# Kernel optimization log

Measured on AMD Instinct MI355X. Metric: run time of the kernel, lower is better.

## Reference

```python
import jax, jax.numpy as jnp
import numpy as np

D = 768
ED = 192  # d // 4
E = 8     # n_experts
K = 2     # top_k
B, H, W = 32, 32, 32
LN_EPS = 1e-5


def setup_inputs() -> dict:
    key = jax.random.key(0)
    ks = jax.random.split(key, 5)
    s = 0.02
    x = jax.random.normal(ks[0], (B, D, H, W), dtype=jnp.float32)
    Wr = jax.random.normal(ks[1], (E, D), dtype=jnp.float32) * s   # router: logits = tokens @ Wr.T
    W1 = jax.random.normal(ks[2], (E, D, ED), dtype=jnp.float32) * s  # gate proj (silu branch)
    W3 = jax.random.normal(ks[3], (E, D, ED), dtype=jnp.float32) * s  # linear branch
    W2 = jax.random.normal(ks[4], (E, ED, D), dtype=jnp.float32) * s  # down proj
    gamma = jnp.ones((D,), dtype=jnp.float32)
    beta = jnp.zeros((D,), dtype=jnp.float32)
    return {"x": x, "Wr": Wr, "W1": W1, "W3": W3, "W2": W2, "gamma": gamma, "beta": beta}


def _layernorm(y, gamma, beta):
    mu = jnp.mean(y, axis=-1, keepdims=True)
    var = jnp.mean(jnp.square(y - mu), axis=-1, keepdims=True)
    return (y - mu) * jax.lax.rsqrt(var + LN_EPS) * gamma + beta


def _moe_forward(x, Wr, W1, W3, W2, gamma, beta):
    b, c, h, w = x.shape
    tokens = x.transpose(0, 2, 3, 1).reshape(-1, c)        # [T, d]
    logits = tokens @ Wr.T                                  # [T, E]
    topk_v, topk_i = jax.lax.top_k(logits, K)               # [T, K]
    topk_w = jax.nn.softmax(topk_v, axis=-1)                # [T, K]
    # dense combine weights: zero for non-selected experts (same math as masked scatter)
    gates = jnp.sum(jax.nn.one_hot(topk_i, E, dtype=tokens.dtype) * topk_w[..., None], axis=1)  # [T, E]
    # SwiGLU per expert (forward uses silu(e[0](t)) * e[2](t), then e[3])
    hdn = jax.nn.silu(jnp.einsum('td,edh->teh', tokens, W1)) * jnp.einsum('td,edh->teh', tokens, W3)  # [T,E,ed]
    y = jnp.einsum('te,teh,ehd->td', gates, hdn, W2)        # combine: [T, d]
    out = _layernorm(y, gamma, beta) + tokens
    return out.reshape(b, h, w, c).transpose(0, 3, 1, 2)


def reference(x, Wr, W1, W3, W2, gamma, beta):
    return _moe_forward(x, Wr, W1, W3, W2, gamma, beta)
```

## Files before the change

kernel.cpp:

```cpp
#include <hip/hip_runtime.h>
#include <cstdint>
#include <cstddef>

#define T_TOK 32768
#define DM 768
#define EDIM 192
#define NEXP 8

typedef unsigned short u16;
typedef short bf16x8 __attribute__((ext_vector_type(8)));
typedef float f32x4 __attribute__((ext_vector_type(4)));
typedef u16 u16x8 __attribute__((ext_vector_type(8)));

__device__ __forceinline__ u16 f2bf(float f) {
  unsigned u = __float_as_uint(f);
  return (u16)((u + 0x7FFFu + ((u >> 16) & 1u)) >> 16);
}
__device__ __forceinline__ float bf2f(u16 u) {
  return __uint_as_float(((unsigned)u) << 16);
}

__device__ __forceinline__ bf16x8 frag_ld(const u16* lds, int row, int kb) {
  int ph = row * 128 + (kb ^ ((row & 7) << 4));
  return *(const bf16x8*)((const char*)lds + ph);
}

__global__ __launch_bounds__(256) void k_prep(
    const float* __restrict__ W1, const float* __restrict__ W3,
    const float* __restrict__ W2, u16* __restrict__ W1T,
    u16* __restrict__ W3T, u16* __restrict__ W2T)
{
  __shared__ __align__(16) float td[64][68];
  const int z = blockIdx.z;
  const int mat = z >> 3, e = z & 7;
  const int R = (mat == 2) ? EDIM : DM;
  const int C = (mat == 2) ? DM : EDIM;
  const int r0 = blockIdx.x * 64, c0 = blockIdx.y * 64;
  if (r0 >= R || c0 >= C) return;
  const float* in = (mat == 0 ? W1 : mat == 1 ? W3 : W2) + (size_t)e * R * C;
  u16* out = (mat == 0 ? W1T : mat == 1 ? W3T : W2T) + (size_t)e * R * C;
  const int tid = threadIdx.x;
  {
    int rl = tid >> 2, cs = (tid & 3) * 16;
    const float* s = in + (size_t)(r0 + rl) * C + c0 + cs;
    #pragma unroll
    for (int i = 0; i < 16; i += 4) *(float4*)&td[rl][cs + i] = *(const float4*)(s + i);
  }
  __syncthreads();
  {
    int cl = tid >> 2, rs = (tid & 3) * 16;
    u16* d = out + (size_t)(c0 + cl) * R + r0 + rs;
    u16x8 o0, o1;
    #pragma unroll
    for (int i = 0; i < 8; ++i) {
      o0[i] = f2bf(td[rs + i][cl]);
      o1[i] = f2bf(td[rs + 8 + i][cl]);
    }
    *(u16x8*)d = o0;
    *(u16x8*)(d + 8) = o1;
  }
}

__global__ __launch_bounds__(256) void k_tokrouter(
    const float* __restrict__ x, const float* __restrict__ Wr,
    u16* __restrict__ tokbf, int* __restrict__ cnt,
    int* __restrict__ toklist, float* __restrict__ gatelist)
{
  __shared__ __align__(16) float tokL[64][64];
  __shared__ float WrL[8][64];
  __shared__ float logitsL[64][8];
  __shared__ int cnt8[8];
  __shared__ int baseL[8];
  const int tid = threadIdx.x;
  const int t0 = blockIdx.x * 64;
  const int b = t0 >> 10;
  const int h0 = (t0 >> 5) & 31;
  const float* xb = x + (size_t)b * (DM * 1024);

  const int tr = tid & 63;
  const int ep = tid >> 6;
  float l0 = 0.f, l1 = 0.f;

  for (int cb = 0; cb < 12; ++cb) {
    const int c0 = cb * 64;
    __syncthreads();
    {
      int f = tid;
      #pragma unroll
      for (int it = 0; it < 2; ++it, f += 256)
        WrL[f >> 6][f & 63] = Wr[(f >> 6) * DM + c0 + (f & 63)];
    }
    {
      int cl = tid >> 2;
      int ts = (tid & 3) * 16;
      int hh = h0 + (ts >> 5), ww = ts & 31;
      const float* src = xb + ((size_t)(c0 + cl) * 32 + hh) * 32 + ww;
      float* d = &tokL[cl][ts];
      #pragma unroll
      for (int i = 0; i < 16; i += 4) *(float4*)(d + i) = *(const float4*)(src + i);
    }
    __syncthreads();
    for (int c = 0; c < 64; ++c) {
      float tv = tokL[c][tr];
      l0 = fmaf(tv, WrL[ep][c], l0);
      l1 = fmaf(tv, WrL[ep + 4][c], l1);
    }
    {
      int tl = tid >> 2;
      int cs = (tid & 3) * 16;
      u16x8 o0, o1;
      #pragma unroll
      for (int i = 0; i < 8; ++i) {
        o0[i] = f2bf(tokL[cs + i][tl]);
        o1[i] = f2bf(tokL[cs + 8 + i][tl]);
      }
      u16* d = tokbf + (size_t)(t0 + tl) * DM + c0 + cs;
      *(u16x8*)d = o0;
      *(u16x8*)(d + 8) = o1;
    }
  }

  logitsL[tr][ep] = l0;
  logitsL[tr][ep + 4] = l1;
  if (tid < 8) cnt8[tid] = 0;
  __syncthreads();

  int e0 = -1, e1 = -1, lp0 = 0, lp1 = 0;
  float g0 = 0.f, g1 = 0.f;
  if (tid < 64) {
    float v0 = -1e30f, v1 = -1e30f;
    #pragma unroll
    for (int e = 0; e < 8; ++e) { float v = logitsL[tid][e]; if (v > v0) { v0 = v; e0 = e; } }
    #pragma unroll
    for (int e = 0; e < 8; ++e) {
      if (e == e0) continue;
      float v = logitsL[tid][e]; if (v > v1) { v1 = v; e1 = e; }
    }
    float w = expf(v1 - v0);
    g0 = 1.f / (1.f + w);
    g1 = w / (1.f + w);
    lp0 = atomicAdd(&cnt8[e0], 1);
    lp1 = atomicAdd(&cnt8[e1], 1);
  }
  __syncthreads();
  if (tid < 8) baseL[tid] = atomicAdd(&cnt[tid], cnt8[tid]);
  __syncthreads();
  if (tid < 64) {
    int tg = t0 + tid;
    int p0 = baseL[e0] + lp0;
    int p1 = baseL[e1] + lp1;
    toklist[e0 * T_TOK + p0] = tg;
    gatelist[e0 * T_TOK + p0] = g0;
    toklist[e1 * T_TOK + p1] = tg | (1 << 16);
    gatelist[e1 * T_TOK + p1] = g1;
  }
}

__global__ void k_prefix(const int* __restrict__ cnt, int* __restrict__ offs) {
  if (threadIdx.x == 0) {
    int s = 0;
    for (int e = 0; e < NEXP; ++e) { offs[e] = s; s += cnt[e]; }
    offs[NEXP] = s;
  }
}

__global__ __launch_bounds__(256) void k_ffn1(
    const u16* __restrict__ tokbf, const u16* __restrict__ W1T,
    const u16* __restrict__ W3T, const int* __restrict__ cnt,
    const int* __restrict__ offs, const int* __restrict__ toklist,
    u16* __restrict__ hbuf)
{
  __shared__ __align__(16) u16 As[128 * 64];
  __shared__ __align__(16) u16 B1s[64 * 64];
  __shared__ __align__(16) u16 B3s[64 * 64];
  __shared__ int rowbaseL[128];
  const int e = blockIdx.z;
  const int count = cnt[e];
  const int start = blockIdx.x * 128;
  if (start >= count) return;
  const int n0 = blockIdx.y * 64;
  const int rows = min(128, count - start);
  const int tid = threadIdx.x;

  if (tid < 128) {
    int r = (tid < rows) ? tid : 0;
    rowbaseL[tid] = (toklist[e * T_TOK + start + r] & 0xFFFF) * DM;
  }
  __syncthreads();

  const int w = tid >> 6, l = tid & 63;
  const int wm = (w >> 1) * 64, wn = (w & 1) * 32;
  const int lr = l & 15;
  const int lk = (l >> 4) * 16;

  f32x4 acc1[4][2], acc3[4][2];
  #pragma unroll
  for (int i = 0; i < 4; ++i)
    #pragma unroll
    for (int j = 0; j < 2; ++j) {
      acc1[i][j] = (f32x4){0.f, 0.f, 0.f, 0.f};
      acc3[i][j] = (f32x4){0.f, 0.f, 0.f, 0.f};
    }

  for (int kc = 0; kc < 12; ++kc) {
    #pragma unroll
    for (int it = 0; it < 4; ++it) {
      int idx = it * 256 + tid;
      int r = idx >> 3, s = idx & 7;
      int sw = (s * 16) ^ ((r & 7) << 4);
      const u16* src = tokbf + rowbaseL[r] + kc * 64 + (sw >> 1);
      *(u16x8*)((char*)As + idx * 16) = *(const u16x8*)src;
    }
    #pragma unroll
    for (int it = 0; it < 2; ++it) {
      int idx = it * 256 + tid;
      int r = idx >> 3, s = idx & 7;
      int sw = (s * 16) ^ ((r & 7) << 4);
      size_t wb = (size_t)(e * EDIM + n0 + r) * DM + kc * 64 + (sw >> 1);
      *(u16x8*)((char*)B1s + idx * 16) = *(const u16x8*)(W1T + wb);
      *(u16x8*)((char*)B3s + idx * 16) = *(const u16x8*)(W3T + wb);
    }
    __syncthreads();
    #pragma unroll
    for (int kk = 0; kk < 2; ++kk) {
      const int kb = kk * 64 + lk;
      bf16x8 af[4], b1[2], b3[2];
      #pragma unroll
      for (int mf = 0; mf < 4; ++mf) af[mf] = frag_ld(As, wm + mf * 16 + lr, kb);
      #pragma unroll
      for (int nf = 0; nf < 2; ++nf) {
        b1[nf] = frag_ld(B1s, wn + nf * 16 + lr, kb);
        b3[nf] = frag_ld(B3s, wn + nf * 16 + lr, kb);
      }
      #pragma unroll
      for (int mf = 0; mf < 4; ++mf)
        #pragma unroll
        for (int nf = 0; nf < 2; ++nf) {
          acc1[mf][nf] = __builtin_amdgcn_mfma_f32_16x16x32_bf16(af[mf], b1[nf], acc1[mf][nf], 0, 0, 0);
          acc3[mf][nf] = __builtin_amdgcn_mfma_f32_16x16x32_bf16(af[mf], b3[nf], acc3[mf][nf], 0, 0, 0);
        }
    }
    __syncthreads();
  }

  const int rq = (l >> 4) * 4;
  const int abase = offs[e] + start;
  #pragma unroll
  for (int mf = 0; mf < 4; ++mf)
    #pragma unroll
    for (int nf = 0; nf < 2; ++nf)
      #pragma unroll
      for (int r = 0; r < 4; ++r) {
        int m = wm + mf * 16 + rq + r;
        if (m < rows) {
          float a = acc1[mf][nf][r];
          float hv = (a / (1.f + expf(-a))) * acc3[mf][nf][r];
          hbuf[(size_t)(abase + m) * EDIM + (n0 + wn + nf * 16 + lr)] = f2bf(hv);
        }
      }
}

__global__ __launch_bounds__(256) void k_ffn2(
    const u16* __restrict__ hbuf, const u16* __restrict__ W2T,
    const int* __restrict__ cnt, const int* __restrict__ offs,
    const int* __restrict__ toklist, const float* __restrict__ gatelist,
    u16* __restrict__ ypart)
{
  __shared__ __align__(16) u16 As[128 * 64];
  __shared__ __align__(16) u16 Bs[128 * 64];
  __shared__ int dstL[128];
  __shared__ float gL[128];
  const int e = blockIdx.z;
  const int count = cnt[e];
  const int start = blockIdx.x * 128;
  if (start >= count) return;
  const int n0 = blockIdx.y * 128;
  const int rows = min(128, count - start);
  const int tid = threadIdx.x;
  const int abase = offs[e] + start;

  if (tid < 128) {
    int r = (tid < rows) ? tid : 0;
    int entry = toklist[e * T_TOK + start + r];
    int t = entry & 0xFFFF, k = entry >> 16;
    dstL[tid] = (k * T_TOK + t) * DM;
    gL[tid] = gatelist[e * T_TOK + start + r];
  }
  __syncthreads();

  const int w = tid >> 6, l = tid & 63;
  const int wm = (w >> 1) * 64, wn = (w & 1) * 64;
  const int lr = l & 15;
  const int lk = (l >> 4) * 16;

  f32x4 acc[4][4];
  #pragma unroll
  for (int i = 0; i < 4; ++i)
    #pragma unroll
    for (int j = 0; j < 4; ++j) acc[i][j] = (f32x4){0.f, 0.f, 0.f, 0.f};

  for (int kc = 0; kc < 3; ++kc) {
    #pragma unroll
    for (int it = 0; it < 4; ++it) {
      int idx = it * 256 + tid;
      int r = idx >> 3, s = idx & 7;
      int sw = (s * 16) ^ ((r & 7) << 4);
      int rr = (r < rows) ? r : 0;
      const u16* sa = hbuf + (size_t)(abase + rr) * EDIM + kc * 64 + (sw >> 1);
      *(u16x8*)((char*)As + idx * 16) = *(const u16x8*)sa;
      const u16* sb = W2T + (size_t)(e * DM + n0 + r) * EDIM + kc * 64 + (sw >> 1);
      *(u16x8*)((char*)Bs + idx * 16) = *(const u16x8*)sb;
    }
    __syncthreads();
    #pragma unroll
    for (int kk = 0; kk < 2; ++kk) {
      const int kb = kk * 64 + lk;
      bf16x8 af[4], bf_[4];
      #pragma unroll
      for (int mf = 0; mf < 4; ++mf) af[mf] = frag_ld(As, wm + mf * 16 + lr, kb);
      #pragma unroll
      for (int nf = 0; nf < 4; ++nf) bf_[nf] = frag_ld(Bs, wn + nf * 16 + lr, kb);
      #pragma unroll
      for (int mf = 0; mf < 4; ++mf)
        #pragma unroll
        for (int nf = 0; nf < 4; ++nf)
          acc[mf][nf] = __builtin_amdgcn_mfma_f32_16x16x32_bf16(af[mf], bf_[nf], acc[mf][nf], 0, 0, 0);
    }
    __syncthreads();
  }

  const int rq = (l >> 4) * 4;
  #pragma unroll
  for (int mf = 0; mf < 4; ++mf)
    #pragma unroll
    for (int nf = 0; nf < 4; ++nf)
      #pragma unroll
      for (int r = 0; r < 4; ++r) {
        int m = wm + mf * 16 + rq + r;
        if (m < rows) {
          float v = acc[mf][nf][r] * gL[m];
          ypart[(size_t)dstL[m] + (n0 + wn + nf * 16 + lr)] = f2bf(v);
        }
      }
}

__global__ __launch_bounds__(256) void k_ln(
    const u16* __restrict__ ypart, const float* __restrict__ x,
    const float* __restrict__ gamma, const float* __restrict__ beta,
    float* __restrict__ out)
{
  __shared__ float lnT[64][65];
  __shared__ float muL[64], rsL[64];
  const int tid = threadIdx.x;
  const int t0 = blockIdx.x * 64;
  const int b = t0 >> 10;
  const int h0 = (t0 >> 5) & 31;
  const u16* y0 = ypart;
  const u16* y1 = ypart + (size_t)T_TOK * DM;
  const int tl = tid >> 2, q = tid & 3;
  const size_t tbase = (size_t)(t0 + tl) * DM;

  float sum = 0.f, sq = 0.f;
  for (int jj = 0; jj < 12; ++jj) {
    int c = jj * 64 + q * 16;
    u16x8 a0 = *(const u16x8*)(y0 + tbase + c);
    u16x8 a1 = *(const u16x8*)(y0 + tbase + c + 8);
    u16x8 b0 = *(const u16x8*)(y1 + tbase + c);
    u16x8 b1 = *(const u16x8*)(y1 + tbase + c + 8);
    #pragma unroll
    for (int i = 0; i < 8; ++i) {
      float v = bf2f(a0[i]) + bf2f(b0[i]); sum += v; sq += v * v;
      float u = bf2f(a1[i]) + bf2f(b1[i]); sum += u; sq += u * u;
    }
  }
  sum += __shfl_xor(sum, 1); sq += __shfl_xor(sq, 1);
  sum += __shfl_xor(sum, 2); sq += __shfl_xor(sq, 2);
  float mu = sum * (1.f / 768.f);
  float var = sq * (1.f / 768.f) - mu * mu;
  float rs = 1.0f / sqrtf(var + 1e-5f);
  if (q == 0) { muL[tl] = mu; rsL[tl] = rs; }
  __syncthreads();

  for (int cb = 0; cb < 12; ++cb) {
    const int c0 = cb * 64;
    if (cb) __syncthreads();
    {
      float mu_ = muL[tl], rs_ = rsL[tl];
      int c = c0 + q * 16;
      u16x8 a0 = *(const u16x8*)(y0 + tbase + c);
      u16x8 a1 = *(const u16x8*)(y0 + tbase + c + 8);
      u16x8 b0 = *(const u16x8*)(y1 + tbase + c);
      u16x8 b1 = *(const u16x8*)(y1 + tbase + c + 8);
      #pragma unroll
      for (int i = 0; i < 8; ++i) {
        float v = bf2f(a0[i]) + bf2f(b0[i]);
        lnT[q * 16 + i][tl] = (v - mu_) * rs_ * gamma[c + i] + beta[c + i];
        float u = bf2f(a1[i]) + bf2f(b1[i]);
        lnT[q * 16 + 8 + i][tl] = (u - mu_) * rs_ * gamma[c + 8 + i] + beta[c + 8 + i];
      }
    }
    __syncthreads();
    {
      int cl = tid >> 2, ts = (tid & 3) * 16;
      int c = c0 + cl;
      int hh = h0 + (ts >> 5), ww = ts & 31;
      size_t oidx = (((size_t)b * DM + c) * 32 + hh) * 32 + ww;
      #pragma unroll
      for (int i = 0; i < 16; i += 4) {
        float4 xv = *(const float4*)(x + oidx + i);
        float4 ov;
        ov.x = lnT[cl][ts + i + 0] + xv.x;
        ov.y = lnT[cl][ts + i + 1] + xv.y;
        ov.z = lnT[cl][ts + i + 2] + xv.z;
        ov.w = lnT[cl][ts + i + 3] + xv.w;
        *(float4*)(out + oidx + i) = ov;
      }
    }
  }
}

constexpr size_t OFF_TOK  = 0;
constexpr size_t OFF_W1T  = OFF_TOK + (size_t)T_TOK * DM * 2;
constexpr size_t OFF_W3T  = OFF_W1T + (size_t)NEXP * EDIM * DM * 2;
constexpr size_t OFF_W2T  = OFF_W3T + (size_t)NEXP * EDIM * DM * 2;
constexpr size_t OFF_H    = OFF_W2T + (size_t)NEXP * EDIM * DM * 2;
constexpr size_t OFF_YP   = OFF_H + (size_t)T_TOK * 2 * EDIM * 2;
constexpr size_t OFF_CNT  = OFF_YP + (size_t)2 * T_TOK * DM * 2;
constexpr size_t OFF_OFFS = OFF_CNT + 256;
constexpr size_t OFF_LIST = OFF_OFFS + 256;
constexpr size_t OFF_GATE = OFF_LIST + (size_t)NEXP * T_TOK * 4;

extern "C" void kernel_launch(void* const* d_in, const int* in_sizes, int n_in,
                              void* d_out, int out_size, void* d_ws, size_t ws_size,
                              hipStream_t stream) {
  const float* x     = (const float*)d_in[0];
  const float* Wr    = (const float*)d_in[1];
  const float* W1    = (const float*)d_in[2];
  const float* W3    = (const float*)d_in[3];
  const float* W2    = (const float*)d_in[4];
  const float* gamma = (const float*)d_in[5];
  const float* beta  = (const float*)d_in[6];
  float* out = (float*)d_out;
  char* ws = (char*)d_ws;

  u16* tokbf = (u16*)(ws + OFF_TOK);
  u16* W1T   = (u16*)(ws + OFF_W1T);
  u16* W3T   = (u16*)(ws + OFF_W3T);
  u16* W2T   = (u16*)(ws + OFF_W2T);
  u16* hbuf  = (u16*)(ws + OFF_H);
  u16* ypart = (u16*)(ws + OFF_YP);
  int* cnt   = (int*)(ws + OFF_CNT);
  int* offs  = (int*)(ws + OFF_OFFS);
  int* toklist = (int*)(ws + OFF_LIST);
  float* gatelist = (float*)(ws + OFF_GATE);

  hipMemsetAsync(cnt, 0, 64, stream);
  hipLaunchKernelGGL(k_prep, dim3(12, 12, 24), dim3(256), 0, stream,
                     W1, W3, W2, W1T, W3T, W2T);
  hipLaunchKernelGGL(k_tokrouter, dim3(512), dim3(256), 0, stream,
                     x, Wr, tokbf, cnt, toklist, gatelist);
  hipLaunchKernelGGL(k_prefix, dim3(1), dim3(64), 0, stream, cnt, offs);
  hipLaunchKernelGGL(k_ffn1, dim3(256, 3, 8), dim3(256), 0, stream,
                     tokbf, W1T, W3T, cnt, offs, toklist, hbuf);
  hipLaunchKernelGGL(k_ffn2, dim3(256, 6, 8), dim3(256), 0, stream,
                     hbuf, W2T, cnt, offs, toklist, gatelist, ypart);
  hipLaunchKernelGGL(k_ln, dim3(512), dim3(256), 0, stream,
                     ypart, x, gamma, beta, out);
}
```

Baseline: 246.6 us.

## Use direct global-to-LDS loads in FFN GEMMs and split router and layernorm for parallelism

The FFN1 and FFN2 GEMM tile loads now use global_load_lds, which writes global memory straight into LDS without passing through registers, and source pointers are computed once outside the k-loop. The router kernel now handles 32 tokens per block (twice as many blocks), keeps all of Wr in LDS, and gives each thread one (token, expert) logit. The layernorm is split into a per-token stats kernel and a 2D-grid apply kernel so more blocks run in parallel. The cost is an extra launch and an extra read of ypart, and the direct LDS loads depend on the swizzled layout matching the lane-ordered writes.

```diff
diff --git a/kernel.cpp b/kernel.cpp
--- a/kernel.cpp
+++ b/kernel.cpp
@@ -18,6 +18,13 @@
 }
 __device__ __forceinline__ float bf2f(u16 u) {
   return __uint_as_float(((unsigned)u) << 16);
+}
+
+__device__ __forceinline__ void gld16(const void* g, void* l) {
+  __builtin_amdgcn_global_load_lds(
+      (const __attribute__((address_space(1))) unsigned int*)g,
+      (__attribute__((address_space(3))) unsigned int*)l,
+      16, 0, 0);
 }
 
 __device__ __forceinline__ bf16x8 frag_ld(const u16* lds, int row, int kb) {
@@ -66,68 +73,58 @@
     u16* __restrict__ tokbf, int* __restrict__ cnt,
     int* __restrict__ toklist, float* __restrict__ gatelist)
 {
-  __shared__ __align__(16) float tokL[64][64];
-  __shared__ float WrL[8][64];
-  __shared__ float logitsL[64][8];
+  __shared__ float WrL[8][772];
+  __shared__ float xL[64][33];
+  __shared__ float logitsL[32][8];
   __shared__ int cnt8[8];
   __shared__ int baseL[8];
   const int tid = threadIdx.x;
-  const int t0 = blockIdx.x * 64;
+  const int t0 = blockIdx.x * 32;
   const int b = t0 >> 10;
-  const int h0 = (t0 >> 5) & 31;
-  const float* xb = x + (size_t)b * (DM * 1024);
-
-  const int tr = tid & 63;
-  const int ep = tid >> 6;
-  float l0 = 0.f, l1 = 0.f;
+  const int h = (t0 >> 5) & 31;
+  const float* xb = x + (size_t)b * (DM * 1024) + h * 32;
+
+  for (int i = tid; i < 1536; i += 256) {
+    int r = i / 192;
+    int c = (i - r * 192) * 4;
+    *(float4*)&WrL[r][c] = ((const float4*)Wr)[i];
+  }
+
+  const int rt = tid >> 3;
+  const int re = tid & 7;
+  float lacc = 0.f;
 
   for (int cb = 0; cb < 12; ++cb) {
     const int c0 = cb * 64;
     __syncthreads();
+    #pragma unroll
+    for (int it = 0; it < 2; ++it) {
+      int idx = it * 256 + tid;
+      int r = idx >> 3, cc = (idx & 7) * 4;
+      float4 v = *(const float4*)(xb + (size_t)(c0 + r) * 1024 + cc);
+      xL[r][cc] = v.x; xL[r][cc + 1] = v.y; xL[r][cc + 2] = v.z; xL[r][cc + 3] = v.w;
+    }
+    __syncthreads();
     {
-      int f = tid;
-      #pragma unroll
-      for (int it = 0; it < 2; ++it, f += 256)
-        WrL[f >> 6][f & 63] = Wr[(f >> 6) * DM + c0 + (f & 63)];
+      const float* wr = &WrL[re][c0];
+      #pragma unroll
+      for (int c = 0; c < 64; ++c) lacc = fmaf(xL[c][rt], wr[c], lacc);
     }
     {
-      int cl = tid >> 2;
-      int ts = (tid & 3) * 16;
-      int hh = h0 + (ts >> 5), ww = ts & 31;
-      const float* src = xb + ((size_t)(c0 + cl) * 32 + hh) * 32 + ww;
-      float* d = &tokL[cl][ts];
-      #pragma unroll
-      for (int i = 0; i < 16; i += 4) *(float4*)(d + i) = *(const float4*)(src + i);
-    }
-    __syncthreads();
-    for (int c = 0; c < 64; ++c) {
-      float tv = tokL[c][tr];
-      l0 = fmaf(tv, WrL[ep][c], l0);
-      l1 = fmaf(tv, WrL[ep + 4][c], l1);
-    }
-    {
-      int tl = tid >> 2;
-      int cs = (tid & 3) * 16;
-      u16x8 o0, o1;
-      #pragma unroll
-      for (int i = 0; i < 8; ++i) {
-        o0[i] = f2bf(tokL[cs + i][tl]);
-        o1[i] = f2bf(tokL[cs + 8 + i][tl]);
-      }
-      u16* d = tokbf + (size_t)(t0 + tl) * DM + c0 + cs;
-      *(u16x8*)d = o0;
-      *(u16x8*)(d + 8) = o1;
-    }
-  }
-
-  logitsL[tr][ep] = l0;
-  logitsL[tr][ep + 4] = l1;
+      u16x8 o;
+      #pragma unroll
+      for (int i = 0; i < 8; ++i) o[i] = f2bf(xL[re * 8 + i][rt]);
+      *(u16x8*)(tokbf + (size_t)(t0 + rt) * DM + c0 + re * 8) = o;
+    }
+  }
+
+  logitsL[rt][re] = lacc;
   if (tid < 8) cnt8[tid] = 0;
   __syncthreads();
 
   int e0 = -1, e1 = -1, lp0 = 0, lp1 = 0;
   float g0 = 0.f, g1 = 0.f;
-  if (tid < 64) {
+  if (tid < 32) {
     float v0 = -1e30f, v1 = -1e30f;
     #pragma unroll
     for (int e = 0; e < 8; ++e) { float v = logitsL[tid][e]; if (v > v0) { v0 = v; e0 = e; } }
@@ -145,7 +142,7 @@
   __syncthreads();
   if (tid < 8) baseL[tid] = atomicAdd(&cnt[tid], cnt8[tid]);
   __syncthreads();
-  if (tid < 64) {
+  if (tid < 32) {
     int tg = t0 + tid;
     int p0 = baseL[e0] + lp0;
     int p1 = baseL[e1] + lp1;
@@ -188,6 +185,19 @@
   }
   __syncthreads();
 
+  const int lrow = tid >> 3;
+  const int swq = (((tid & 7) * 16) ^ ((lrow & 7) << 4)) >> 1;
+  const u16 *srcA[4], *srcB1[2], *srcB3[2];
+  #pragma unroll
+  for (int it = 0; it < 4; ++it)
+    srcA[it] = tokbf + rowbaseL[it * 32 + lrow] + swq;
+  #pragma unroll
+  for (int it = 0; it < 2; ++it) {
+    size_t wb = (size_t)(e * EDIM + n0 + it * 32 + lrow) * DM + swq;
+    srcB1[it] = W1T + wb;
+    srcB3[it] = W3T + wb;
+  }
+
   const int w = tid >> 6, l = tid & 63;
   const int wm = (w >> 1) * 64, wn = (w & 1) * 32;
   const int lr = l & 15;
@@ -203,22 +213,14 @@
     }
 
   for (int kc = 0; kc < 12; ++kc) {
-    #pragma unroll
-    for (int it = 0; it < 4; ++it) {
-      int idx = it * 256 + tid;
-      int r = idx >> 3, s = idx & 7;
-      int sw = (s * 16) ^ ((r & 7) << 4);
-      const u16* src = tokbf + rowbaseL[r] + kc * 64 + (sw >> 1);
-      *(u16x8*)((char*)As + idx * 16) = *(const u16x8*)src;
-    }
+    const int ko = kc * 64;
+    #pragma unroll
+    for (int it = 0; it < 4; ++it)
+      gld16(srcA[it] + ko, (char*)As + (it * 256 + tid) * 16);
     #pragma unroll
     for (int it = 0; it < 2; ++it) {
-      int idx = it * 256 + tid;
-      int r = idx >> 3, s = idx & 7;
-      int sw = (s * 16) ^ ((r & 7) << 4);
-      size_t wb = (size_t)(e * EDIM + n0 + r) * DM + kc * 64 + (sw >> 1);
-      *(u16x8*)((char*)B1s + idx * 16) = *(const u16x8*)(W1T + wb);
-      *(u16x8*)((char*)B3s + idx * 16) = *(const u16x8*)(W3T + wb);
+      gld16(srcB1[it] + ko, (char*)B1s + (it * 256 + tid) * 16);
+      gld16(srcB3[it] + ko, (char*)B3s + (it * 256 + tid) * 16);
     }
     __syncthreads();
     #pragma unroll
@@ -288,6 +290,17 @@
   }
   __syncthreads();
 
+  const int lrow = tid >> 3;
+  const int swq = (((tid & 7) * 16) ^ ((lrow & 7) << 4)) >> 1;
+  const u16 *srcA[4], *srcB[4];
+  #pragma unroll
+  for (int it = 0; it < 4; ++it) {
+    int r = it * 32 + lrow;
+    int rr = (r < rows) ? r : 0;
+    srcA[it] = hbuf + (size_t)(abase + rr) * EDIM + swq;
+    srcB[it] = W2T + (size_t)(e * DM + n0 + r) * EDIM + swq;
+  }
+
   const int w = tid >> 6, l = tid & 63;
   const int wm = (w >> 1) * 64, wn = (w & 1) * 64;
   const int lr = l & 15;
@@ -300,16 +313,11 @@
     for (int j = 0; j < 4; ++j) acc[i][j] = (f32x4){0.f, 0.f, 0.f, 0.f};
 
   for (int kc = 0; kc < 3; ++kc) {
+    const int ko = kc * 64;
     #pragma unroll
     for (int it = 0; it < 4; ++it) {
-      int idx = it * 256 + tid;
-      int r = idx >> 3, s = idx & 7;
-      int sw = (s * 16) ^ ((r & 7) << 4);
-      int rr = (r < rows) ? r : 0;
-      const u16* sa = hbuf + (size_t)(abase + rr) * EDIM + kc * 64 + (sw >> 1);
-      *(u16x8*)((char*)As + idx * 16) = *(const u16x8*)sa;
-      const u16* sb = W2T + (size_t)(e * DM + n0 + r) * EDIM + kc * 64 + (sw >> 1);
-      *(u16x8*)((char*)Bs + idx * 16) = *(const u16x8*)sb;
+      gld16(srcA[it] + ko, (char*)As + (it * 256 + tid) * 16);
+      gld16(srcB[it] + ko, (char*)Bs + (it * 256 + tid) * 16);
     }
     __syncthreads();
     #pragma unroll
@@ -344,77 +352,82 @@
       }
 }
 
-__global__ __launch_bounds__(256) void k_ln(
+__global__ __launch_bounds__(256) void k_stats(
+    const u16* __restrict__ ypart, float* __restrict__ mu, float* __restrict__ rs)
+{
+  const int tid = threadIdx.x;
+  const int t = blockIdx.x * 16 + (tid >> 4);
+  const int j = tid & 15;
+  const u16* y0 = ypart + (size_t)t * DM;
+  const u16* y1 = y0 + (size_t)T_TOK * DM;
+  float sum = 0.f, sq = 0.f;
+  #pragma unroll
+  for (int i = 0; i < 6; ++i) {
+    int c = i * 128 + j * 8;
+    u16x8 a = *(const u16x8*)(y0 + c);
+    u16x8 b = *(const u16x8*)(y1 + c);
+    #pragma unroll
+    for (int q = 0; q < 8; ++q) {
+      float v = bf2f(a[q]) + bf2f(b[q]);
+      sum += v; sq += v * v;
+    }
+  }
+  #pragma unroll
+  for (int d = 1; d < 16; d <<= 1) { sum += __shfl_xor(sum, d); sq += __shfl_xor(sq, d); }
+  if (j == 0) {
+    float m = sum * (1.f / 768.f);
+    float var = sq * (1.f / 768.f) - m * m;
+    mu[t] = m;
+    rs[t] = 1.f / sqrtf(var + 1e-5f);
+  }
+}
+
+__global__ __launch_bounds__(256) void k_apply(
     const u16* __restrict__ ypart, const float* __restrict__ x,
     const float* __restrict__ gamma, const float* __restrict__ beta,
+    const float* __restrict__ mu, const float* __restrict__ rs,
     float* __restrict__ out)
 {
   __shared__ float lnT[64][65];
-  __shared__ float muL[64], rsL[64];
   const int tid = threadIdx.x;
   const int t0 = blockIdx.x * 64;
+  const int c0 = blockIdx.y * 64;
   const int b = t0 >> 10;
   const int h0 = (t0 >> 5) & 31;
   const u16* y0 = ypart;
   const u16* y1 = ypart + (size_t)T_TOK * DM;
-  const int tl = tid >> 2, q = tid & 3;
-  const size_t tbase = (size_t)(t0 + tl) * DM;
-
-  float sum = 0.f, sq = 0.f;
-  for (int jj = 0; jj < 12; ++jj) {
-    int c = jj * 64 + q * 16;
+  {
+    const int tl = tid >> 2, q = tid & 3;
+    const size_t tbase = (size_t)(t0 + tl) * DM;
+    const int c = c0 + q * 16;
+    const float mu_ = mu[t0 + tl], rs_ = rs[t0 + tl];
     u16x8 a0 = *(const u16x8*)(y0 + tbase + c);
     u16x8 a1 = *(const u16x8*)(y0 + tbase + c + 8);
     u16x8 b0 = *(const u16x8*)(y1 + tbase + c);
     u16x8 b1 = *(const u16x8*)(y1 + tbase + c + 8);
     #pragma unroll
     for (int i = 0; i < 8; ++i) {
-      float v = bf2f(a0[i]) + bf2f(b0[i]); sum += v; sq += v * v;
-      float u = bf2f(a1[i]) + bf2f(b1[i]); sum += u; sq += u * u;
-    }
-  }
-  sum += __shfl_xor(sum, 1); sq += __shfl_xor(sq, 1);
-  sum += __shfl_xor(sum, 2); sq += __shfl_xor(sq, 2);
-  float mu = sum * (1.f / 768.f);
-  float var = sq * (1.f / 768.f) - mu * mu;
-  float rs = 1.0f / sqrtf(var + 1e-5f);
-  if (q == 0) { muL[tl] = mu; rsL[tl] = rs; }
-  __syncthreads();
-
-  for (int cb = 0; cb < 12; ++cb) {
-    const int c0 = cb * 64;
-    if (cb) __syncthreads();
-    {
-      float mu_ = muL[tl], rs_ = rsL[tl];
-      int c = c0 + q * 16;
-      u16x8 a0 = *(const u16x8*)(y0 + tbase + c);
-      u16x8 a1 = *(const u16x8*)(y0 + tbase + c + 8);
-      u16x8 b0 = *(const u16x8*)(y1 + tbase + c);
-      u16x8 b1 = *(const u16x8*)(y1 + tbase + c + 8);
-      #pragma unroll
-      for (int i = 0; i < 8; ++i) {
-        float v = bf2f(a0[i]) + bf2f(b0[i]);
-        lnT[q * 16 + i][tl] = (v - mu_) * rs_ * gamma[c + i] + beta[c + i];
-        float u = bf2f(a1[i]) + bf2f(b1[i]);
-        lnT[q * 16 + 8 + i][tl] = (u - mu_) * rs_ * gamma[c + 8 + i] + beta[c + 8 + i];
-      }
-    }
-    __syncthreads();
-    {
-      int cl = tid >> 2, ts = (tid & 3) * 16;
-      int c = c0 + cl;
-      int hh = h0 + (ts >> 5), ww = ts & 31;
-      size_t oidx = (((size_t)b * DM + c) * 32 + hh) * 32 + ww;
-      #pragma unroll
-      for (int i = 0; i < 16; i += 4) {
-        float4 xv = *(const float4*)(x + oidx + i);
-        float4 ov;
-        ov.x = lnT[cl][ts + i + 0] + xv.x;
-        ov.y = lnT[cl][ts + i + 1] + xv.y;
-        ov.z = lnT[cl][ts + i + 2] + xv.z;
-        ov.w = lnT[cl][ts + i + 3] + xv.w;
-        *(float4*)(out + oidx + i) = ov;
-      }
+      float v = bf2f(a0[i]) + bf2f(b0[i]);
+      lnT[q * 16 + i][tl] = (v - mu_) * rs_ * gamma[c + i] + beta[c + i];
+      float u = bf2f(a1[i]) + bf2f(b1[i]);
+      lnT[q * 16 + 8 + i][tl] = (u - mu_) * rs_ * gamma[c + 8 + i] + beta[c + 8 + i];
+    }
+  }
+  __syncthreads();
+  {
+    int cl = tid >> 2, ts = (tid & 3) * 16;
+    int c = c0 + cl;
+    int hh = h0 + (ts >> 5), ww = ts & 31;
+    size_t oidx = (((size_t)b * DM + c) * 32 + hh) * 32 + ww;
+    #pragma unroll
+    for (int i = 0; i < 16; i += 4) {
+      float4 xv = *(const float4*)(x + oidx + i);
+      float4 ov;
+      ov.x = lnT[cl][ts + i + 0] + xv.x;
+      ov.y = lnT[cl][ts + i + 1] + xv.y;
+      ov.z = lnT[cl][ts + i + 2] + xv.z;
+      ov.w = lnT[cl][ts + i + 3] + xv.w;
+      *(float4*)(out + oidx + i) = ov;
     }
   }
 }
@@ -429,6 +442,8 @@
 constexpr size_t OFF_OFFS = OFF_CNT + 256;
 constexpr size_t OFF_LIST = OFF_OFFS + 256;
 constexpr size_t OFF_GATE = OFF_LIST + (size_t)NEXP * T_TOK * 4;
+constexpr size_t OFF_MU   = OFF_GATE + (size_t)NEXP * T_TOK * 4;
+constexpr size_t OFF_RS   = OFF_MU + (size_t)T_TOK * 4;
 
 extern "C" void kernel_launch(void* const* d_in, const int* in_sizes, int n_in,
                               void* d_out, int out_size, void* d_ws, size_t ws_size,
@@ -453,17 +468,21 @@
   int* offs  = (int*)(ws + OFF_OFFS);
   int* toklist = (int*)(ws + OFF_LIST);
   float* gatelist = (float*)(ws + OFF_GATE);
+  float* muB = (float*)(ws + OFF_MU);
+  float* rsB = (float*)(ws + OFF_RS);
 
   hipMemsetAsync(cnt, 0, 64, stream);
   hipLaunchKernelGGL(k_prep, dim3(12, 12, 24), dim3(256), 0, stream,
                      W1, W3, W2, W1T, W3T, W2T);
-  hipLaunchKernelGGL(k_tokrouter, dim3(512), dim3(256), 0, stream,
+  hipLaunchKernelGGL(k_tokrouter, dim3(1024), dim3(256), 0, stream,
                      x, Wr, tokbf, cnt, toklist, gatelist);
   hipLaunchKernelGGL(k_prefix, dim3(1), dim3(64), 0, stream, cnt, offs);
   hipLaunchKernelGGL(k_ffn1, dim3(256, 3, 8), dim3(256), 0, stream,
                      tokbf, W1T, W3T, cnt, offs, toklist, hbuf);
   hipLaunchKernelGGL(k_ffn2, dim3(256, 6, 8), dim3(256), 0, stream,
                      hbuf, W2T, cnt, offs, toklist, gatelist, ypart);
-  hipLaunchKernelGGL(k_ln, dim3(512), dim3(256), 0, stream,
-                     ypart, x, gamma, beta, out);
-}
+  hipLaunchKernelGGL(k_stats, dim3(2048), dim3(256), 0, stream,
+                     ypart, muB, rsB);
+  hipLaunchKernelGGL(k_apply, dim3(512, 12), dim3(256), 0, stream,
+                     ypart, x, gamma, beta, muB, rsB, out);
+}
```

Measured after the change: 238.3 us. 3.3% less time.
